# Performance work log

Measured on AMD Instinct MI355X. Metric: run time of the kernel, lower is better.

## Reference

```python
import jax, jax.numpy as jnp
import numpy as np

B, T, E = 2, 2048, 2048
H, HKV, D = 32, 8, 64
G = H // HKV  # groups = 4
ROPE_BASE = 10000.0


def setup_inputs() -> dict:
    key = jax.random.key(0)
    ks = jax.random.split(key, 5)
    s = 0.02
    return {
        "x": jax.random.normal(ks[0], (B, T, E), dtype=jnp.float32),
        "Wq": jax.random.normal(ks[1], (E, H * D), dtype=jnp.float32) * s,
        "Wk": jax.random.normal(ks[2], (E, HKV * D), dtype=jnp.float32) * s,
        "Wv": jax.random.normal(ks[3], (E, HKV * D), dtype=jnp.float32) * s,
        "Wo": jax.random.normal(ks[4], (E, E), dtype=jnp.float32) * s,
    }


def _rope_tables(t, d, dtype):
    # standard rotate-half RoPE, theta base 10000
    inv_freq = 1.0 / (ROPE_BASE ** (jnp.arange(0, d, 2, dtype=jnp.float32) / d))
    ang = jnp.arange(t, dtype=jnp.float32)[:, None] * inv_freq[None, :]  # [T, D/2]
    return jnp.cos(ang).astype(dtype), jnp.sin(ang).astype(dtype)


def _apply_rope(x, cos, sin):
    # x: [B, h, T, D]; cos/sin: [T, D/2]
    d2 = x.shape[-1] // 2
    x1, x2 = x[..., :d2], x[..., d2:]
    return jnp.concatenate([x1 * cos - x2 * sin, x2 * cos + x1 * sin], axis=-1)


def reference(x, Wq, Wk, Wv, Wo):
    b, t, _ = x.shape
    q = (x @ Wq).reshape(b, t, H, D).transpose(0, 2, 1, 3)      # [B,H,T,D]
    k = (x @ Wk).reshape(b, t, HKV, D).transpose(0, 2, 1, 3)    # [B,HKV,T,D]
    v = (x @ Wv).reshape(b, t, HKV, D).transpose(0, 2, 1, 3)    # [B,HKV,T,D]

    cos, sin = _rope_tables(t, D, x.dtype)
    q = _apply_rope(q, cos, sin)
    k = _apply_rope(k, cos, sin)

    # GQA: keep KV unexpanded, broadcast groups inside the contraction
    qg = q.reshape(b, HKV, G, t, D)
    scale = 1.0 / np.sqrt(D)
    scores = jnp.einsum('bkgtd,bksd->bkgts', qg, k) * scale      # [B,HKV,G,T,T]
    causal = jnp.tril(jnp.ones((t, t), dtype=bool))
    scores = jnp.where(causal, scores, jnp.finfo(scores.dtype).min)
    attn = jax.nn.softmax(scores, axis=-1)
    y = jnp.einsum('bkgts,bksd->bkgtd', attn, v)                 # [B,HKV,G,T,D]
    y = y.reshape(b, H, t, D).transpose(0, 2, 1, 3).reshape(b, t, H * D)
    return y @ Wo
```

## Files before the change

kernel.cpp:

```cpp
#include <hip/hip_runtime.h>
#include <hip/hip_bf16.h>
#include <cstdint>
#include <cstddef>

typedef __bf16 bf16;
typedef __attribute__((ext_vector_type(8))) __bf16 bf16x8;
typedef __attribute__((ext_vector_type(4))) __bf16 bf16x4v;
typedef __attribute__((ext_vector_type(4))) float f32x4;

#define NB 2
#define NT 2048
#define NE 2048
#define NH 32
#define NHKV 8
#define ND 64
#define NBT (NB * NT)
#define NQKV 3072

__device__ __forceinline__ void gload_lds16(const void* g, void* l) {
  __builtin_amdgcn_global_load_lds(
      (const __attribute__((address_space(1))) unsigned int*)g,
      (__attribute__((address_space(3))) unsigned int*)l, 16, 0, 0);
}

__device__ __forceinline__ int swz(int row, int byteoff) {
  return (row * 128 + byteoff) ^ ((row & 7) << 4);
}


__global__ void cvt_bf16_kernel(const float* __restrict__ in, bf16* __restrict__ out, int n4) {
  int i = blockIdx.x * blockDim.x + threadIdx.x;
  const int stride = gridDim.x * blockDim.x;
  for (; i < n4; i += stride) {
    const float4 v = ((const float4*)in)[i];
    bf16x4v o;
    o[0] = (bf16)v.x; o[1] = (bf16)v.y; o[2] = (bf16)v.z; o[3] = (bf16)v.w;
    ((bf16x4v*)out)[i] = o;
  }
}

__global__ void transpose_cvt_kernel(const float* __restrict__ in, bf16* __restrict__ out,
                                     int ncols, int rowoff) {
  __shared__ float tile[32][33];
  const int c0 = blockIdx.x * 32;
  const int k0 = blockIdx.y * 32;
  const int tx = threadIdx.x, ty = threadIdx.y;
#pragma unroll
  for (int j = 0; j < 4; ++j)
    tile[ty + j * 8][tx] = in[(size_t)(k0 + ty + j * 8) * ncols + c0 + tx];
  __syncthreads();
#pragma unroll
  for (int j = 0; j < 4; ++j)
    out[(size_t)(rowoff + c0 + ty + j * 8) * 2048 + k0 + tx] = (bf16)tile[tx][ty + j * 8];
}

__global__ void rope_table_kernel(float* __restrict__ tab) {
  int i = blockIdx.x * 256 + threadIdx.x;
  if (i >= NT * 32) return;
  const int t = i >> 5, d = i & 31;
  const float inv = expf(-(float)d * 0.28782313662425574f);
  const float ang = (float)t * inv;
  tab[t * 64 + d] = cosf(ang);
  tab[t * 64 + 32 + d] = sinf(ang);
}

__global__ void build_vt_kernel(const bf16* __restrict__ qkv, bf16* __restrict__ vt) {
  __shared__ bf16 tile[32][33];
  const int bhk = blockIdx.z;
  const int b = bhk >> 3, hk = bhk & 7;
  const int d0 = blockIdx.x * 32, t0 = blockIdx.y * 32;
  const int tx = threadIdx.x, ty = threadIdx.y;
#pragma unroll
  for (int j = 0; j < 4; ++j)
    tile[ty + j * 8][tx] = qkv[(size_t)(b * NT + t0 + ty + j * 8) * NQKV + 2560 + hk * 64 + d0 + tx];
  __syncthreads();
#pragma unroll
  for (int j = 0; j < 4; ++j)
    vt[((size_t)(b * NHKV + hk) * 64 + d0 + ty + j * 8) * NT + t0 + tx] = tile[tx][ty + j * 8];
}


template <typename CT, bool ROPE>
__global__ __launch_bounds__(256, 3)
void gemm_r3_kernel(const bf16* __restrict__ A, const bf16* __restrict__ Bt,
                    CT* __restrict__ C, int M, int N, int K,
                    const float* __restrict__ tab) {
  __shared__ __align__(16) bf16 As[3][128 * 32];
  __shared__ __align__(16) bf16 Bs[3][128 * 32];
  const int tid = threadIdx.x;
  const int lane = tid & 63, wid = tid >> 6;
  const int wr = wid >> 1, wc = wid & 1;
  const int cpx = (int)gridDim.x >> 3;
  const int swzb = ((int)blockIdx.x & 7) * cpx + ((int)blockIdx.x >> 3);
  const int gx = N >> 7;
  const int bx = swzb % gx, by = swzb / gx;
  const int m0 = by * 128, n0 = bx * 128;
  const int srow = tid >> 2;
  const int skoff = (tid & 3) * 8;
  const bf16* ga = A + (size_t)(m0 + srow) * K + skoff;
  const bf16* gb = Bt + (size_t)(n0 + srow) * K + skoff;
  const int fr = lane & 15;
  const int fk = (lane >> 4) * 8;
  const int NTK = K >> 5;
  f32x4 acc[4][4] = {};

#define STAGE_T(b, t)                                                   \
  do {                                                                  \
    const int kk = (t) * 32;                                            \
    gload_lds16(ga + kk, &As[b][tid * 8]);                              \
    gload_lds16(ga + kk + (size_t)64 * K, &As[b][2048 + tid * 8]);      \
    gload_lds16(gb + kk, &Bs[b][tid * 8]);                              \
    gload_lds16(gb + kk + (size_t)64 * K, &Bs[b][2048 + tid * 8]);      \
  } while (0)

  STAGE_T(0, 0);
  STAGE_T(1, 1);

  int bc = 0;
  for (int t = 0; t < NTK; ++t) {
    if (t + 1 < NTK) asm volatile("s_waitcnt vmcnt(4)" ::: "memory");
    else             asm volatile("s_waitcnt vmcnt(0)" ::: "memory");
    __builtin_amdgcn_s_barrier();

    bf16x8 af[4], bfr[4];
#pragma unroll
    for (int m = 0; m < 4; ++m)
      af[m] = *(const bf16x8*)&As[bc][(wr * 64 + m * 16 + fr) * 32 + fk];
#pragma unroll
    for (int n = 0; n < 4; ++n)
      bfr[n] = *(const bf16x8*)&Bs[bc][(wc * 64 + n * 16 + fr) * 32 + fk];

    if (t + 2 < NTK) {
      const int pb = (bc + 2 >= 3) ? bc - 1 : bc + 2;
      STAGE_T(pb, t + 2);
    }

    __builtin_amdgcn_s_setprio(1);
#pragma unroll
    for (int m = 0; m < 4; ++m)
#pragma unroll
      for (int n = 0; n < 4; ++n)
        acc[m][n] = __builtin_amdgcn_mfma_f32_16x16x32_bf16(af[m], bfr[n], acc[m][n], 0, 0, 0);
    __builtin_amdgcn_s_setprio(0);
    bc = (bc + 1 == 3) ? 0 : bc + 1;
  }
#undef STAGE_T

  const int colbase = n0 + wc * 64;
  const bool do_rope = ROPE && colbase < 2560;
  const bool do_scale = ROPE && colbase < 2048;
  const float SCALE = 0.18033688011112042f;
  const int orow0 = m0 + wr * 64 + (lane >> 4) * 4;
  const int ocol0 = colbase + fr;
#pragma unroll
  for (int m = 0; m < 4; ++m) {
#pragma unroll
    for (int j = 0; j < 4; ++j) {
      const int row = orow0 + m * 16 + j;
      float v0 = acc[m][0][j], v1 = acc[m][1][j], v2 = acc[m][2][j], v3 = acc[m][3][j];
      if (do_rope) {
        const int tt = row & (NT - 1);
        const float c0 = tab[tt * 64 + fr],      s0 = tab[tt * 64 + 32 + fr];
        const float c1 = tab[tt * 64 + 16 + fr], s1 = tab[tt * 64 + 48 + fr];
        const float a0 = v0, a2 = v2;
        v0 = a0 * c0 - a2 * s0;
        v2 = a2 * c0 + a0 * s0;
        const float a1 = v1, a3 = v3;
        v1 = a1 * c1 - a3 * s1;
        v3 = a3 * c1 + a1 * s1;
        if (do_scale) { v0 *= SCALE; v1 *= SCALE; v2 *= SCALE; v3 *= SCALE; }
      }
      CT* cp = &C[(size_t)row * N + ocol0];
      cp[0] = (CT)v0; cp[16] = (CT)v1; cp[32] = (CT)v2; cp[48] = (CT)v3;
    }
  }
}


__global__ __launch_bounds__(256, 3)
void attn_kernel(const bf16* __restrict__ qkv, const bf16* __restrict__ vt,
                 bf16* __restrict__ y) {
  const int bid = blockIdx.x;
  const int qtb = 15 - (bid >> 6);
  const int bh = bid & 63;
  const int b = bh >> 5, h = bh & 31, hk = h >> 2;
  const int q0 = qtb * 128;

  __shared__ __align__(16) bf16 Kb[3][4096], Vb[3][4096];

  const int tid = threadIdx.x;
  const int lane = tid & 63, wid = tid >> 6;
  const int ql = lane & 15;
  const int sub = lane >> 4;

  const int st_r = tid >> 3;
  const int kperm = 4 * (st_r >> 4) + 8 * ((st_r >> 2) & 3) + (st_r & 3);
  const int csw = ((tid & 7) ^ (st_r & 7)) * 8;
  const bf16* kgbase = qkv + (size_t)(b * NT + kperm) * NQKV + 2048 + hk * 64 + csw;
  const bf16* vgbase = vt + ((size_t)(b * NHKV + hk) * 64 + st_r) * NT + csw;

  auto STAGE = [&](int buf, int kv0) {
    const bf16* kg = kgbase + (size_t)kv0 * NQKV;
    gload_lds16(kg, Kb[buf] + tid * 8);
    gload_lds16(kg + (size_t)32 * NQKV, Kb[buf] + 2048 + tid * 8);
    const bf16* vg = vgbase + kv0;
    gload_lds16(vg, Vb[buf] + tid * 8);
    gload_lds16(vg + 32 * NT, Vb[buf] + 2048 + tid * 8);
  };

  bf16x8 qf[2][2];
#pragma unroll
  for (int set = 0; set < 2; ++set) {
    const bf16* qp = qkv + (size_t)(b * NT + q0 + wid * 32 + set * 16 + ql) * NQKV + h * 64 + sub * 8;
    qf[set][0] = *(const bf16x8*)qp;
    qf[set][1] = *(const bf16x8*)(qp + 32);
  }

  f32x4 o[2][4] = {};
  float m_s[2] = {-1e30f, -1e30f};
  float l_s[2] = {0.f, 0.f};

  const int ntiles = 2 * qtb + 2;
  STAGE(0, 0);
  STAGE(1, 64);

  int bc = 0;
  for (int it = 0; it < ntiles; ++it) {
    const int kv0 = it * 64;
    if (it + 1 < ntiles) asm volatile("s_waitcnt vmcnt(4)" ::: "memory");
    else                 asm volatile("s_waitcnt vmcnt(0)" ::: "memory");
    __builtin_amdgcn_s_barrier();

    if (it + 2 < ntiles) {
      const int pb = (bc + 2 >= 3) ? bc - 1 : bc + 2;
      STAGE(pb, kv0 + 128);
    }

    if (kv0 <= q0 + wid * 32 + 47) {
      bf16x8 kf[4][2];
#pragma unroll
      for (int n = 0; n < 4; ++n)
#pragma unroll
        for (int c = 0; c < 2; ++c)
          kf[n][c] = *(const bf16x8*)((const char*)Kb[bc] + swz(n * 16 + ql, c * 64 + sub * 16));
      bf16x8 vf[2][4];
#pragma unroll
      for (int kc = 0; kc < 2; ++kc)
#pragma unroll
        for (int dt = 0; dt < 4; ++dt)
          vf[kc][dt] = *(const bf16x8*)((const char*)Vb[bc] + swz(dt * 16 + ql, kc * 64 + sub * 16));

#pragma unroll
      for (int set = 0; set < 2; ++set) {
        const int qlo = q0 + wid * 32 + set * 16;
        if (kv0 > qlo + 15) continue;

        f32x4 s[4] = {};
        __builtin_amdgcn_s_setprio(1);
#pragma unroll
        for (int n = 0; n < 4; ++n) {
          s[n] = __builtin_amdgcn_mfma_f32_16x16x32_bf16(kf[n][0], qf[set][0], s[n], 0, 0, 0);
          s[n] = __builtin_amdgcn_mfma_f32_16x16x32_bf16(kf[n][1], qf[set][1], s[n], 0, 0, 0);
        }
        __builtin_amdgcn_s_setprio(0);

        float p[4][4];
        if (kv0 + 63 > qlo) {
          const int qrow = qlo + ql;
#pragma unroll
          for (int n = 0; n < 4; ++n) {
            const int kvb = kv0 + 32 * (n >> 1) + 4 * (n & 1) + 8 * sub;
#pragma unroll
            for (int j = 0; j < 4; ++j)
              p[n][j] = (kvb + j > qrow) ? -1e30f : s[n][j];
          }
        } else {
#pragma unroll
          for (int n = 0; n < 4; ++n)
#pragma unroll
            for (int j = 0; j < 4; ++j)
              p[n][j] = s[n][j];
        }

        float rmax = p[0][0];
#pragma unroll
        for (int n = 0; n < 4; ++n)
#pragma unroll
          for (int j = 0; j < 4; ++j) rmax = fmaxf(rmax, p[n][j]);
        rmax = fmaxf(rmax, __shfl_xor(rmax, 16));
        rmax = fmaxf(rmax, __shfl_xor(rmax, 32));

        if (!__all(rmax <= m_s[set] + 8.0f)) {
          const float mnew = fmaxf(m_s[set], rmax);
          const float sc = exp2f(m_s[set] - mnew);
          m_s[set] = mnew;
          l_s[set] *= sc;
#pragma unroll
          for (int dt = 0; dt < 4; ++dt) o[set][dt] *= sc;
        }
        const float mcur = m_s[set];

        float rsum = 0.f;
        bf16x8 pb2[2];
#pragma unroll
        for (int n = 0; n < 4; ++n)
#pragma unroll
          for (int j = 0; j < 4; ++j) {
            const float e = exp2f(p[n][j] - mcur);
            rsum += e;
            pb2[n >> 1][(n & 1) * 4 + j] = (bf16)e;
          }
        rsum += __shfl_xor(rsum, 16);
        rsum += __shfl_xor(rsum, 32);
        l_s[set] += rsum;

        __builtin_amdgcn_s_setprio(1);
#pragma unroll
        for (int kc = 0; kc < 2; ++kc)
#pragma unroll
          for (int dt = 0; dt < 4; ++dt)
            o[set][dt] = __builtin_amdgcn_mfma_f32_16x16x32_bf16(vf[kc][dt], pb2[kc], o[set][dt], 0, 0, 0);
        __builtin_amdgcn_s_setprio(0);
      }
    }
    bc = (bc + 1 == 3) ? 0 : bc + 1;
  }

#pragma unroll
  for (int set = 0; set < 2; ++set) {
    const float inv = 1.0f / l_s[set];
    bf16* yp = y + (size_t)(b * NT + q0 + wid * 32 + set * 16 + ql) * NE + h * 64 + sub * 4;
#pragma unroll
    for (int dt = 0; dt < 4; ++dt) {
      bf16x4v w;
      w[0] = (bf16)(o[set][dt][0] * inv);
      w[1] = (bf16)(o[set][dt][1] * inv);
      w[2] = (bf16)(o[set][dt][2] * inv);
      w[3] = (bf16)(o[set][dt][3] * inv);
      *(bf16x4v*)(yp + dt * 16) = w;
    }
  }
}


extern "C" void kernel_launch(void* const* d_in, const int* in_sizes, int n_in,
                              void* d_out, int out_size, void* d_ws, size_t ws_size,
                              hipStream_t stream) {
  const float* x = (const float*)d_in[0];
  const float* Wq = (const float*)d_in[1];
  const float* Wk = (const float*)d_in[2];
  const float* Wv = (const float*)d_in[3];
  const float* Wo = (const float*)d_in[4];
  float* out = (float*)d_out;

  char* ws = (char*)d_ws;
  size_t off = 0;
  auto alloc = [&](size_t bytes) -> void* {
    void* p = ws + off;
    off += (bytes + 255) & ~(size_t)255;
    return p;
  };
  bf16* xb = (bf16*)alloc((size_t)NBT * NE * 2);
  bf16* wqkv_t = (bf16*)alloc((size_t)NQKV * NE * 2);
  bf16* wo_t = (bf16*)alloc((size_t)NE * NE * 2);
  bf16* qkv = (bf16*)alloc((size_t)NBT * NQKV * 2);
  bf16* vtb = (bf16*)alloc((size_t)NB * NHKV * ND * NT * 2);
  bf16* yb = (bf16*)alloc((size_t)NBT * NE * 2);
  float* tab = (float*)alloc((size_t)NT * 64 * 4);

  cvt_bf16_kernel<<<2048, 256, 0, stream>>>(x, xb, NBT * NE / 4);
  dim3 tb(32, 8);
  transpose_cvt_kernel<<<dim3(64, 64), tb, 0, stream>>>(Wq, wqkv_t, 2048, 0);
  transpose_cvt_kernel<<<dim3(16, 64), tb, 0, stream>>>(Wk, wqkv_t, 512, 2048);
  transpose_cvt_kernel<<<dim3(16, 64), tb, 0, stream>>>(Wv, wqkv_t, 512, 2560);
  transpose_cvt_kernel<<<dim3(64, 64), tb, 0, stream>>>(Wo, wo_t, 2048, 0);
  rope_table_kernel<<<(NT * 32 + 255) / 256, 256, 0, stream>>>(tab);

  gemm_r3_kernel<bf16, true><<<dim3((NQKV / 128) * (NBT / 128)), 256, 0, stream>>>(
      xb, wqkv_t, qkv, NBT, NQKV, NE, tab);
  build_vt_kernel<<<dim3(2, 64, 16), tb, 0, stream>>>(qkv, vtb);
  attn_kernel<<<dim3(NT / 128 * 64), 256, 0, stream>>>(qkv, vtb, yb);
  gemm_r3_kernel<float, false><<<dim3((NE / 128) * (NBT / 128)), 256, 0, stream>>>(
      yb, wo_t, out, NBT, NE, NE, nullptr);
}
```

Baseline: 204.6 us.

## Fuse V transpose into QKV GEMM, swizzle LDS, compute row sums via MFMA

The QKV GEMM epilogue now writes V tiles straight into the transposed V buffer, so the separate build_vt kernel and its extra global round-trip go away. The GEMM's LDS staging and fragment reads use an XOR swizzle on the k-offset to cut bank conflicts. The attention softmax denominator is now accumulated by an extra MFMA against a vector of ones instead of scalar sums plus cross-lane shuffles. The row sum is then built from bf16-rounded probabilities, which changes numerics slightly. The QKV GEMM also gets a branchy epilogue with strided writes.

```diff
diff --git a/kernel.cpp b/kernel.cpp
--- a/kernel.cpp
+++ b/kernel.cpp
@@ -64,27 +64,12 @@
   tab[t * 64 + 32 + d] = sinf(ang);
 }
 
-__global__ void build_vt_kernel(const bf16* __restrict__ qkv, bf16* __restrict__ vt) {
-  __shared__ bf16 tile[32][33];
-  const int bhk = blockIdx.z;
-  const int b = bhk >> 3, hk = bhk & 7;
-  const int d0 = blockIdx.x * 32, t0 = blockIdx.y * 32;
-  const int tx = threadIdx.x, ty = threadIdx.y;
-#pragma unroll
-  for (int j = 0; j < 4; ++j)
-    tile[ty + j * 8][tx] = qkv[(size_t)(b * NT + t0 + ty + j * 8) * NQKV + 2560 + hk * 64 + d0 + tx];
-  __syncthreads();
-#pragma unroll
-  for (int j = 0; j < 4; ++j)
-    vt[((size_t)(b * NHKV + hk) * 64 + d0 + ty + j * 8) * NT + t0 + tx] = tile[tx][ty + j * 8];
-}
-
 
 template <typename CT, bool ROPE>
 __global__ __launch_bounds__(256, 3)
 void gemm_r3_kernel(const bf16* __restrict__ A, const bf16* __restrict__ Bt,
                     CT* __restrict__ C, int M, int N, int K,
-                    const float* __restrict__ tab) {
+                    const float* __restrict__ tab, bf16* __restrict__ vt) {
   __shared__ __align__(16) bf16 As[3][128 * 32];
   __shared__ __align__(16) bf16 Bs[3][128 * 32];
   const int tid = threadIdx.x;
@@ -96,11 +81,12 @@
   const int bx = swzb % gx, by = swzb / gx;
   const int m0 = by * 128, n0 = bx * 128;
   const int srow = tid >> 2;
-  const int skoff = (tid & 3) * 8;
+  const int skoff = 8 * ((tid & 3) ^ ((tid >> 3) & 3));
   const bf16* ga = A + (size_t)(m0 + srow) * K + skoff;
   const bf16* gb = Bt + (size_t)(n0 + srow) * K + skoff;
   const int fr = lane & 15;
-  const int fk = (lane >> 4) * 8;
+  const int fq = lane >> 4;
+  const int fks = 8 * (fq ^ ((fr >> 1) & 3));
   const int NTK = K >> 5;
   f32x4 acc[4][4] = {};
 
@@ -125,10 +111,10 @@
     bf16x8 af[4], bfr[4];
 #pragma unroll
     for (int m = 0; m < 4; ++m)
-      af[m] = *(const bf16x8*)&As[bc][(wr * 64 + m * 16 + fr) * 32 + fk];
+      af[m] = *(const bf16x8*)&As[bc][(wr * 64 + m * 16 + fr) * 32 + fks];
 #pragma unroll
     for (int n = 0; n < 4; ++n)
-      bfr[n] = *(const bf16x8*)&Bs[bc][(wc * 64 + n * 16 + fr) * 32 + fk];
+      bfr[n] = *(const bf16x8*)&Bs[bc][(wc * 64 + n * 16 + fr) * 32 + fks];
 
     if (t + 2 < NTK) {
       const int pb = (bc + 2 >= 3) ? bc - 1 : bc + 2;
@@ -147,10 +133,32 @@
 #undef STAGE_T
 
   const int colbase = n0 + wc * 64;
+
+  if (ROPE && colbase >= 2560) {
+    const int hk = (colbase - 2560) >> 6;
+    const int bb = m0 >> 11;
+    const int t0 = (m0 & (NT - 1)) + wr * 64 + fq * 4;
+    bf16* vtp = vt + (size_t)(bb * NHKV + hk) * 64 * NT;
+#pragma unroll
+    for (int m = 0; m < 4; ++m) {
+#pragma unroll
+      for (int n = 0; n < 4; ++n) {
+        const int d = n * 16 + fr;
+        bf16x4v w;
+        w[0] = (bf16)acc[m][n][0];
+        w[1] = (bf16)acc[m][n][1];
+        w[2] = (bf16)acc[m][n][2];
+        w[3] = (bf16)acc[m][n][3];
+        *(bf16x4v*)&vtp[(size_t)d * NT + t0 + m * 16] = w;
+      }
+    }
+    return;
+  }
+
   const bool do_rope = ROPE && colbase < 2560;
   const bool do_scale = ROPE && colbase < 2048;
   const float SCALE = 0.18033688011112042f;
-  const int orow0 = m0 + wr * 64 + (lane >> 4) * 4;
+  const int orow0 = m0 + wr * 64 + fq * 4;
   const int ocol0 = colbase + fr;
 #pragma unroll
   for (int m = 0; m < 4; ++m) {
@@ -216,9 +224,13 @@
     qf[set][1] = *(const bf16x8*)(qp + 32);
   }
 
+  bf16x8 ones8;
+#pragma unroll
+  for (int i = 0; i < 8; ++i) ones8[i] = (bf16)1.0f;
+
   f32x4 o[2][4] = {};
+  f32x4 ol[2] = {};
   float m_s[2] = {-1e30f, -1e30f};
-  float l_s[2] = {0.f, 0.f};
 
   const int ntiles = 2 * qtb + 2;
   STAGE(0, 0);
@@ -294,32 +306,27 @@
           const float mnew = fmaxf(m_s[set], rmax);
           const float sc = exp2f(m_s[set] - mnew);
           m_s[set] = mnew;
-          l_s[set] *= sc;
+          ol[set] *= sc;
 #pragma unroll
           for (int dt = 0; dt < 4; ++dt) o[set][dt] *= sc;
         }
         const float mcur = m_s[set];
 
-        float rsum = 0.f;
         bf16x8 pb2[2];
 #pragma unroll
         for (int n = 0; n < 4; ++n)
 #pragma unroll
-          for (int j = 0; j < 4; ++j) {
-            const float e = exp2f(p[n][j] - mcur);
-            rsum += e;
-            pb2[n >> 1][(n & 1) * 4 + j] = (bf16)e;
-          }
-        rsum += __shfl_xor(rsum, 16);
-        rsum += __shfl_xor(rsum, 32);
-        l_s[set] += rsum;
+          for (int j = 0; j < 4; ++j)
+            pb2[n >> 1][(n & 1) * 4 + j] = (bf16)exp2f(p[n][j] - mcur);
 
         __builtin_amdgcn_s_setprio(1);
 #pragma unroll
-        for (int kc = 0; kc < 2; ++kc)
+        for (int kc = 0; kc < 2; ++kc) {
+          ol[set] = __builtin_amdgcn_mfma_f32_16x16x32_bf16(ones8, pb2[kc], ol[set], 0, 0, 0);
 #pragma unroll
           for (int dt = 0; dt < 4; ++dt)
             o[set][dt] = __builtin_amdgcn_mfma_f32_16x16x32_bf16(vf[kc][dt], pb2[kc], o[set][dt], 0, 0, 0);
+        }
         __builtin_amdgcn_s_setprio(0);
       }
     }
@@ -328,7 +335,7 @@
 
 #pragma unroll
   for (int set = 0; set < 2; ++set) {
-    const float inv = 1.0f / l_s[set];
+    const float inv = 1.0f / ol[set][0];
     bf16* yp = y + (size_t)(b * NT + q0 + wid * 32 + set * 16 + ql) * NE + h * 64 + sub * 4;
 #pragma unroll
     for (int dt = 0; dt < 4; ++dt) {
@@ -377,9 +384,8 @@
   rope_table_kernel<<<(NT * 32 + 255) / 256, 256, 0, stream>>>(tab);
 
   gemm_r3_kernel<bf16, true><<<dim3((NQKV / 128) * (NBT / 128)), 256, 0, stream>>>(
-      xb, wqkv_t, qkv, NBT, NQKV, NE, tab);
-  build_vt_kernel<<<dim3(2, 64, 16), tb, 0, stream>>>(qkv, vtb);
+      xb, wqkv_t, qkv, NBT, NQKV, NE, tab, vtb);
   attn_kernel<<<dim3(NT / 128 * 64), 256, 0, stream>>>(qkv, vtb, yb);
   gemm_r3_kernel<float, false><<<dim3((NE / 128) * (NBT / 128)), 256, 0, stream>>>(
-      yb, wo_t, out, NBT, NE, NE, nullptr);
-}
+      yb, wo_t, out, NBT, NE, NE, nullptr, nullptr);
+}
```

Measured after the change: 199.5 us. 2.5% less time.
